# Kernel tuning notes

Measured on AMD Instinct MI355X. Metric: run time of the kernel, lower is better.

Reference implementation:

```python
import jax, jax.numpy as jnp
import numpy as np

T, D, H, O = 1048576, 64, 128, 32  # tokens, input_size, expert hidden, expert output_size


def setup_inputs() -> dict:
    key = jax.random.key(0)
    ks = jax.random.split(key, 11)
    s = 0.02
    return {
        "x": jax.random.normal(ks[0], (T, D), dtype=jnp.float32),
        "topk_idx": jax.random.randint(ks[1], (T, 2), 0, 2),
        "weights": jax.random.uniform(ks[2], (T, 2), dtype=jnp.float32),
        # expert 0: MLP D -> H -> O
        "W0a": jax.random.normal(ks[3], (D, H), dtype=jnp.float32) * s,
        "b0a": jnp.zeros((H,), dtype=jnp.float32),
        "W0b": jax.random.normal(ks[4], (H, O), dtype=jnp.float32) * s,
        "b0b": jnp.zeros((O,), dtype=jnp.float32),
        # expert 1: MLP (D + O) -> H -> O  (memory-enhanced input)
        "W1a": jax.random.normal(ks[5], (D + O, H), dtype=jnp.float32) * s,
        "b1a": jnp.zeros((H,), dtype=jnp.float32),
        "W1b": jax.random.normal(ks[6], (H, O), dtype=jnp.float32) * s,
        "b1b": jnp.zeros((O,), dtype=jnp.float32),
    }


def reference(x, topk_idx, weights, W0a, b0a, W0b, b0b, W1a, b1a, W1b, b1b):
    mask0 = (topk_idx == 0).any(axis=1)  # [T]
    mask1 = (topk_idx == 1).any(axis=1)  # [T]

    # expert 0 output, zero where not routed (matches zeros buffer + masked scatter)
    e0 = jnp.maximum(x @ W0a + b0a, 0.0) @ W0b + b0b      # [T, O]
    out0 = jnp.where(mask0[:, None], e0, 0.0)

    # last_valid_fill: forward-fill last valid row index (invalid -> 0, then cummax)
    t = jnp.arange(T)
    idx = jax.lax.cummax(jnp.where(mask0, t, 0))           # [T] int
    filled = out0[idx]                                     # [T, O] gather rows

    # expert 1 on [x, last_valid_out0], zero where not routed
    x1 = jnp.concatenate([x, filled], axis=1)              # [T, D+O]
    e1 = jnp.maximum(x1 @ W1a + b1a, 0.0) @ W1b + b1b      # [T, O]
    out1 = jnp.where(mask1[:, None], e1, 0.0)

    w = weights[:, :1]                                     # [T, 1]
    return w * out0 + (1.0 - w) * out1
```

## Files before the change

kernel.cpp:

```cpp
#include <hip/hip_runtime.h>
#include <hip/hip_bf16.h>

#define TROWS 1048576
#define RPC   256
#define CPB   8
#define NBLK  (TROWS / (RPC * CPB))
#define LSTRIDE 36

typedef float f32x4  __attribute__((ext_vector_type(4)));
typedef short bf16x8 __attribute__((ext_vector_type(8)));
typedef short bf16x4 __attribute__((ext_vector_type(4)));

#define MFMA(a, b, c) __builtin_amdgcn_mfma_f32_16x16x32_bf16(a, b, c, 0, 0, 0)

__device__ __forceinline__ short f2bf(float v) {
    __hip_bfloat16 b = __float2bfloat16(v);
    return __builtin_bit_cast(short, b);
}
__device__ __forceinline__ float bf2f(short s) {
    unsigned u = ((unsigned)(unsigned short)s) << 16;
    return __builtin_bit_cast(float, u);
}

__global__ __launch_bounds__(64) void prep_kernel(
    const float* __restrict__ W0a, const float* __restrict__ W0b,
    const float* __restrict__ W1a, const float* __restrict__ W1b,
    bf16x8* __restrict__ frag)
{
    const int fid = blockIdx.x, l = threadIdx.x, c = l & 15, g = l >> 4;
    const float* W; int N, ks, nt;
    if (fid < 16)      { W = W0a; N = 128; ks = fid >> 3;        nt = fid & 7; }
    else if (fid < 24) { W = W0b; N = 32;  ks = (fid - 16) >> 1; nt = (fid - 16) & 1; }
    else if (fid < 48) { W = W1a; N = 128; ks = (fid - 24) >> 3; nt = (fid - 24) & 7; }
    else               { W = W1b; N = 32;  ks = (fid - 48) >> 1; nt = (fid - 48) & 1; }
    bf16x8 f;
    #pragma unroll
    for (int j = 0; j < 8; ++j) {
        const int k = 32 * ks + ((j < 4) ? (4 * g + j) : (16 + 4 * g + (j - 4)));
        f[j] = f2bf(W[k * N + 16 * nt + c]);
    }
    frag[fid * 64 + l] = f;
}

__global__ __launch_bounds__(256, 2) void fused_kernel(
    const float* __restrict__ x, const int* __restrict__ topk,
    const float* __restrict__ wts,
    const float* __restrict__ b0a, const float* __restrict__ b0b,
    const float* __restrict__ b1a, const float* __restrict__ b1b,
    const bf16x8* __restrict__ frag,
    float* __restrict__ out)
{
    const int tid = threadIdx.x, wv = tid >> 6, l = tid & 63, c = l & 15, g = l >> 4;
    const int blk0 = blockIdx.x * (RPC * CPB);

    __shared__ __align__(16) short frag_lds[56 * 64 * 8];
    __shared__ __align__(16) short out0_lds[257 * LSTRIDE];
    __shared__ int wtot[4];

    #define LDSF(fid_) (*(const bf16x8*)&frag_lds[(((fid_) * 64) + l) * 8])

    #pragma unroll
    for (int i = 0; i < 14; ++i)
        *(f32x4*)&frag_lds[(tid + i * 256) * 8] = *(const f32x4*)&frag[tid + i * 256];

    bf16x8 xfp[2];
    bool m0p = false;
    if (wv == 3) {
        int p = 0;
        for (int base = blk0 - 64; base >= 0; base -= 64) {
            const int2 tkq = ((const int2*)topk)[base + l];
            const bool mm = (tkq.x == 0) || (tkq.y == 0);
            const unsigned long long bal = __ballot(mm);
            if (bal) { p = base + 63 - __clzll(bal); break; }
        }
        const int2 tkp = ((const int2*)topk)[p];
        m0p = (tkp.x == 0) || (tkp.y == 0);
        const float* xp = x + (size_t)p * 64;
        #pragma unroll
        for (int ks = 0; ks < 2; ++ks) {
            f32x4 a  = *(const f32x4*)(xp + 32 * ks + 4 * g);
            f32x4 b2 = *(const f32x4*)(xp + 32 * ks + 16 + 4 * g);
            #pragma unroll
            for (int j = 0; j < 4; ++j) { xfp[ks][j] = f2bf(a[j]); xfp[ks][4 + j] = f2bf(b2[j]); }
        }
    }

    f32x4 xraw[16];
    #pragma unroll
    for (int rt = 0; rt < 4; ++rt) {
        const float* xr = x + (size_t)(blk0 + wv * 64 + rt * 16 + c) * 64;
        xraw[rt * 4 + 0] = *(const f32x4*)(xr + 4 * g);
        xraw[rt * 4 + 1] = *(const f32x4*)(xr + 16 + 4 * g);
        xraw[rt * 4 + 2] = *(const f32x4*)(xr + 32 + 4 * g);
        xraw[rt * 4 + 3] = *(const f32x4*)(xr + 48 + 4 * g);
    }
    int2  tko = ((const int2*)topk)[blk0 + tid];
    float wgt = wts[(size_t)(blk0 + tid) * 2];

    __syncthreads();

    if (wv == 3) {
        f32x4 accp0 = *(const f32x4*)(b0b + 4 * g);
        f32x4 accp1 = *(const f32x4*)(b0b + 16 + 4 * g);
        #pragma unroll 1
        for (int k2 = 0; k2 < 4; ++k2) {
            const bf16x8 fa00 = LDSF(0 * 8 + 2 * k2 + 0);
            const bf16x8 fa01 = LDSF(0 * 8 + 2 * k2 + 1);
            const bf16x8 fa10 = LDSF(1 * 8 + 2 * k2 + 0);
            const bf16x8 fa11 = LDSF(1 * 8 + 2 * k2 + 1);
            const bf16x8 fb0  = LDSF(16 + 2 * k2 + 0);
            const bf16x8 fb1  = LDSF(16 + 2 * k2 + 1);
            f32x4 a10 = *(const f32x4*)(b0a + 16 * (2 * k2 + 0) + 4 * g);
            f32x4 a11 = *(const f32x4*)(b0a + 16 * (2 * k2 + 1) + 4 * g);
            a10 = MFMA(fa00, xfp[0], a10);
            a10 = MFMA(fa10, xfp[1], a10);
            a11 = MFMA(fa01, xfp[0], a11);
            a11 = MFMA(fa11, xfp[1], a11);
            bf16x8 hf;
            #pragma unroll
            for (int j = 0; j < 8; ++j)
                hf[j] = f2bf(fmaxf((j < 4 ? a10 : a11)[j & 3], 0.0f));
            accp0 = MFMA(fb0, hf, accp0);
            accp1 = MFMA(fb1, hf, accp1);
        }
        if (c == 0) {
            #pragma unroll
            for (int ot = 0; ot < 2; ++ot) {
                bf16x4 v;
                #pragma unroll
                for (int j = 0; j < 4; ++j)
                    v[j] = f2bf(m0p ? (ot ? accp1[j] : accp0[j]) : 0.0f);
                *(bf16x4*)(&out0_lds[256 * LSTRIDE + 16 * ot + 4 * g]) = v;
            }
        }
    }

    #pragma unroll 1
    for (int ch = 0; ch < CPB; ++ch) {
        const int cb = blk0 + ch * RPC;

        bf16x8 xf[4][2];
        #pragma unroll
        for (int rt = 0; rt < 4; ++rt)
            #pragma unroll
            for (int ks = 0; ks < 2; ++ks) {
                const f32x4 a  = xraw[rt * 4 + ks * 2 + 0];
                const f32x4 b2 = xraw[rt * 4 + ks * 2 + 1];
                #pragma unroll
                for (int j = 0; j < 4; ++j) { xf[rt][ks][j] = f2bf(a[j]); xf[rt][ks][4 + j] = f2bf(b2[j]); }
            }

        const bool m0o = (tko.x == 0) || (tko.y == 0);
        int s = m0o ? (cb + tid) : 0;
        #pragma unroll
        for (int off = 1; off < 64; off <<= 1) {
            int u = __shfl_up(s, off, 64);
            if (l >= off) s = max(s, u);
        }
        if (l == 63) wtot[wv] = s;

        f32x4 acc2a[4][2];
        {
            f32x4 bi0 = *(const f32x4*)(b0b + 4 * g);
            f32x4 bi1 = *(const f32x4*)(b0b + 16 + 4 * g);
            #pragma unroll
            for (int rt = 0; rt < 4; ++rt) { acc2a[rt][0] = bi0; acc2a[rt][1] = bi1; }
        }
        #pragma unroll 1
        for (int k2 = 0; k2 < 4; ++k2) {
            const bf16x8 fa00 = LDSF(0 * 8 + 2 * k2 + 0);
            const bf16x8 fa01 = LDSF(0 * 8 + 2 * k2 + 1);
            const bf16x8 fa10 = LDSF(1 * 8 + 2 * k2 + 0);
            const bf16x8 fa11 = LDSF(1 * 8 + 2 * k2 + 1);
            const bf16x8 fb0  = LDSF(16 + 2 * k2 + 0);
            const bf16x8 fb1  = LDSF(16 + 2 * k2 + 1);
            const f32x4 bi0 = *(const f32x4*)(b0a + 16 * (2 * k2 + 0) + 4 * g);
            const f32x4 bi1 = *(const f32x4*)(b0a + 16 * (2 * k2 + 1) + 4 * g);
            #pragma unroll
            for (int rt = 0; rt < 4; ++rt) {
                f32x4 a10 = bi0, a11 = bi1;
                a10 = MFMA(fa00, xf[rt][0], a10);
                a10 = MFMA(fa10, xf[rt][1], a10);
                a11 = MFMA(fa01, xf[rt][0], a11);
                a11 = MFMA(fa11, xf[rt][1], a11);
                bf16x8 hf;
                #pragma unroll
                for (int j = 0; j < 8; ++j)
                    hf[j] = f2bf(fmaxf((j < 4 ? a10 : a11)[j & 3], 0.0f));
                acc2a[rt][0] = MFMA(fb0, hf, acc2a[rt][0]);
                acc2a[rt][1] = MFMA(fb1, hf, acc2a[rt][1]);
            }
        }

        #pragma unroll
        for (int rt = 0; rt < 4; ++rt) {
            const int slot = wv * 64 + rt * 16 + c;
            const int2 tk = ((const int2*)topk)[cb + slot];
            const bool m0 = (tk.x == 0) || (tk.y == 0);
            #pragma unroll
            for (int ot = 0; ot < 2; ++ot) {
                bf16x4 v;
                #pragma unroll
                for (int j = 0; j < 4; ++j) v[j] = f2bf(m0 ? acc2a[rt][ot][j] : 0.0f);
                *(bf16x4*)(&out0_lds[slot * LSTRIDE + 16 * ot + 4 * g]) = v;
            }
        }

        __syncthreads();

        if (ch + 1 < CPB) {
            const int nb = cb + RPC;
            #pragma unroll
            for (int rt = 0; rt < 4; ++rt) {
                const float* xr = x + (size_t)(nb + wv * 64 + rt * 16 + c) * 64;
                xraw[rt * 4 + 0] = *(const f32x4*)(xr + 4 * g);
                xraw[rt * 4 + 1] = *(const f32x4*)(xr + 16 + 4 * g);
                xraw[rt * 4 + 2] = *(const f32x4*)(xr + 32 + 4 * g);
                xraw[rt * 4 + 3] = *(const f32x4*)(xr + 48 + 4 * g);
            }
            tko = ((const int2*)topk)[nb + tid];
            wgt = wts[(size_t)(nb + tid) * 2];
        }

        int pre = 0;
        #pragma unroll
        for (int w2 = 0; w2 < 4; ++w2)
            if (w2 < wv) pre = max(pre, wtot[w2]);
        const int s_full = max(pre, s);

        bf16x8 xf2[4];
        #pragma unroll
        for (int rt = 0; rt < 4; ++rt) {
            const int sF = __shfl(s_full, rt * 16 + c, 64);
            const int slot = (sF >= cb) ? (sF - cb) : 256;
            const short* fr = &out0_lds[slot * LSTRIDE];
            bf16x4 fa_ = *(const bf16x4*)(fr + 4 * g);
            bf16x4 fb_ = *(const bf16x4*)(fr + 16 + 4 * g);
            #pragma unroll
            for (int j = 0; j < 4; ++j) { xf2[rt][j] = fa_[j]; xf2[rt][4 + j] = fb_[j]; }
        }

        f32x4 acc2b[4][2];
        {
            f32x4 bi0 = *(const f32x4*)(b1b + 4 * g);
            f32x4 bi1 = *(const f32x4*)(b1b + 16 + 4 * g);
            #pragma unroll
            for (int rt = 0; rt < 4; ++rt) { acc2b[rt][0] = bi0; acc2b[rt][1] = bi1; }
        }
        #pragma unroll 1
        for (int k2 = 0; k2 < 4; ++k2) {
            const bf16x8 fa00 = LDSF(24 + 0 * 8 + 2 * k2 + 0);
            const bf16x8 fa01 = LDSF(24 + 0 * 8 + 2 * k2 + 1);
            const bf16x8 fa10 = LDSF(24 + 1 * 8 + 2 * k2 + 0);
            const bf16x8 fa11 = LDSF(24 + 1 * 8 + 2 * k2 + 1);
            const bf16x8 fa20 = LDSF(24 + 2 * 8 + 2 * k2 + 0);
            const bf16x8 fa21 = LDSF(24 + 2 * 8 + 2 * k2 + 1);
            const bf16x8 fb0  = LDSF(48 + 2 * k2 + 0);
            const bf16x8 fb1  = LDSF(48 + 2 * k2 + 1);
            const f32x4 bi0 = *(const f32x4*)(b1a + 16 * (2 * k2 + 0) + 4 * g);
            const f32x4 bi1 = *(const f32x4*)(b1a + 16 * (2 * k2 + 1) + 4 * g);
            #pragma unroll
            for (int rt = 0; rt < 4; ++rt) {
                f32x4 a10 = bi0, a11 = bi1;
                a10 = MFMA(fa00, xf[rt][0], a10);
                a10 = MFMA(fa10, xf[rt][1], a10);
                a10 = MFMA(fa20, xf2[rt], a10);
                a11 = MFMA(fa01, xf[rt][0], a11);
                a11 = MFMA(fa11, xf[rt][1], a11);
                a11 = MFMA(fa21, xf2[rt], a11);
                bf16x8 hf;
                #pragma unroll
                for (int j = 0; j < 8; ++j)
                    hf[j] = f2bf(fmaxf((j < 4 ? a10 : a11)[j & 3], 0.0f));
                acc2b[rt][0] = MFMA(fb0, hf, acc2b[rt][0]);
                acc2b[rt][1] = MFMA(fb1, hf, acc2b[rt][1]);
            }
        }

        #pragma unroll
        for (int rt = 0; rt < 4; ++rt) {
            const int slot = wv * 64 + rt * 16 + c;
            const int row = cb + slot;
            const int2 tk = ((const int2*)topk)[row];
            const bool m1 = (tk.x == 1) || (tk.y == 1);
            const float w  = wts[(size_t)row * 2];
            const float wc = 1.0f - w;
            #pragma unroll
            for (int ot = 0; ot < 2; ++ot) {
                bf16x4 oa = *(const bf16x4*)(&out0_lds[slot * LSTRIDE + 16 * ot + 4 * g]);
                f32x4 r;
                #pragma unroll
                for (int j = 0; j < 4; ++j) {
                    const float e1 = m1 ? acc2b[rt][ot][j] : 0.0f;
                    r[j] = w * bf2f(oa[j]) + wc * e1;
                }
                *(f32x4*)(out + (size_t)row * 32 + 16 * ot + 4 * g) = r;
            }
        }

        uint2 pc; bool docopy = false;
        if (ch + 1 < CPB && wv == 3) {
            const int pn = __shfl(s_full, 63, 64);
            docopy = (pn >= cb);
            if (docopy && l < 8)
                pc = *(const uint2*)&out0_lds[(pn - cb) * LSTRIDE + l * 4];
        }

        __syncthreads();

        if (docopy && l < 8)
            *(uint2*)&out0_lds[256 * LSTRIDE + l * 4] = pc;
    }
    #undef LDSF
}

extern "C" void kernel_launch(void* const* d_in, const int* in_sizes, int n_in,
                              void* d_out, int out_size, void* d_ws, size_t ws_size,
                              hipStream_t stream)
{
    const float* x    = (const float*)d_in[0];
    const int*   topk = (const int*)  d_in[1];
    const float* wts  = (const float*)d_in[2];
    const float* W0a  = (const float*)d_in[3];
    const float* b0a  = (const float*)d_in[4];
    const float* W0b  = (const float*)d_in[5];
    const float* b0b  = (const float*)d_in[6];
    const float* W1a  = (const float*)d_in[7];
    const float* b1a  = (const float*)d_in[8];
    const float* W1b  = (const float*)d_in[9];
    const float* b1b  = (const float*)d_in[10];
    float* out = (float*)d_out;

    bf16x8* frag = (bf16x8*)d_ws;

    prep_kernel<<<dim3(56), dim3(64), 0, stream>>>(W0a, W0b, W1a, W1b, frag);
    fused_kernel<<<dim3(NBLK), dim3(256), 0, stream>>>(
        x, topk, wts, b0a, b0b, b1a, b1b, frag, out);
}
```

Before: 129.1 us.

## Use 512-thread blocks with 32 rows per wave and drop register prefetch

```diff
diff --git a/kernel.cpp b/kernel.cpp
--- a/kernel.cpp
+++ b/kernel.cpp
@@ -42,7 +42,7 @@
     frag[fid * 64 + l] = f;
 }
 
-__global__ __launch_bounds__(256, 2) void fused_kernel(
+__global__ __launch_bounds__(512, 4) void fused_kernel(
     const float* __restrict__ x, const int* __restrict__ topk,
     const float* __restrict__ wts,
     const float* __restrict__ b0a, const float* __restrict__ b0b,
@@ -51,21 +51,22 @@
     float* __restrict__ out)
 {
     const int tid = threadIdx.x, wv = tid >> 6, l = tid & 63, c = l & 15, g = l >> 4;
+    const int rr = l & 31;
     const int blk0 = blockIdx.x * (RPC * CPB);
 
     __shared__ __align__(16) short frag_lds[56 * 64 * 8];
     __shared__ __align__(16) short out0_lds[257 * LSTRIDE];
-    __shared__ int wtot[4];
+    __shared__ int wtot[8];
 
     #define LDSF(fid_) (*(const bf16x8*)&frag_lds[(((fid_) * 64) + l) * 8])
 
     #pragma unroll
-    for (int i = 0; i < 14; ++i)
-        *(f32x4*)&frag_lds[(tid + i * 256) * 8] = *(const f32x4*)&frag[tid + i * 256];
+    for (int i = 0; i < 7; ++i)
+        *(f32x4*)&frag_lds[(tid + i * 512) * 8] = *(const f32x4*)&frag[tid + i * 512];
 
     bf16x8 xfp[2];
     bool m0p = false;
-    if (wv == 3) {
+    if (wv == 7) {
         int p = 0;
         for (int base = blk0 - 64; base >= 0; base -= 64) {
             const int2 tkq = ((const int2*)topk)[base + l];
@@ -85,21 +86,9 @@
         }
     }
 
-    f32x4 xraw[16];
-    #pragma unroll
-    for (int rt = 0; rt < 4; ++rt) {
-        const float* xr = x + (size_t)(blk0 + wv * 64 + rt * 16 + c) * 64;
-        xraw[rt * 4 + 0] = *(const f32x4*)(xr + 4 * g);
-        xraw[rt * 4 + 1] = *(const f32x4*)(xr + 16 + 4 * g);
-        xraw[rt * 4 + 2] = *(const f32x4*)(xr + 32 + 4 * g);
-        xraw[rt * 4 + 3] = *(const f32x4*)(xr + 48 + 4 * g);
-    }
-    int2  tko = ((const int2*)topk)[blk0 + tid];
-    float wgt = wts[(size_t)(blk0 + tid) * 2];
-
     __syncthreads();
 
-    if (wv == 3) {
+    if (wv == 7) {
         f32x4 accp0 = *(const f32x4*)(b0b + 4 * g);
         f32x4 accp1 = *(const f32x4*)(b0b + 16 + 4 * g);
         #pragma unroll 1
@@ -139,32 +128,36 @@
     for (int ch = 0; ch < CPB; ++ch) {
         const int cb = blk0 + ch * RPC;
 
-        bf16x8 xf[4][2];
-        #pragma unroll
-        for (int rt = 0; rt < 4; ++rt)
+        bf16x8 xf[2][2];
+        #pragma unroll
+        for (int rt = 0; rt < 2; ++rt) {
+            const float* xr = x + (size_t)(cb + wv * 32 + rt * 16 + c) * 64;
             #pragma unroll
             for (int ks = 0; ks < 2; ++ks) {
-                const f32x4 a  = xraw[rt * 4 + ks * 2 + 0];
-                const f32x4 b2 = xraw[rt * 4 + ks * 2 + 1];
+                f32x4 a  = *(const f32x4*)(xr + 32 * ks + 4 * g);
+                f32x4 b2 = *(const f32x4*)(xr + 32 * ks + 16 + 4 * g);
                 #pragma unroll
                 for (int j = 0; j < 4; ++j) { xf[rt][ks][j] = f2bf(a[j]); xf[rt][ks][4 + j] = f2bf(b2[j]); }
             }
-
+        }
+
+        const int srow = cb + wv * 32 + rr;
+        const int2 tko = ((const int2*)topk)[srow];
         const bool m0o = (tko.x == 0) || (tko.y == 0);
-        int s = m0o ? (cb + tid) : 0;
-        #pragma unroll
-        for (int off = 1; off < 64; off <<= 1) {
-            int u = __shfl_up(s, off, 64);
-            if (l >= off) s = max(s, u);
-        }
-        if (l == 63) wtot[wv] = s;
-
-        f32x4 acc2a[4][2];
+        int s = m0o ? srow : 0;
+        #pragma unroll
+        for (int off = 1; off < 32; off <<= 1) {
+            int u = __shfl_up(s, off, 32);
+            if (rr >= off) s = max(s, u);
+        }
+        if (l == 31) wtot[wv] = s;
+
+        f32x4 acc2a[2][2];
         {
             f32x4 bi0 = *(const f32x4*)(b0b + 4 * g);
             f32x4 bi1 = *(const f32x4*)(b0b + 16 + 4 * g);
-            #pragma unroll
-            for (int rt = 0; rt < 4; ++rt) { acc2a[rt][0] = bi0; acc2a[rt][1] = bi1; }
+            acc2a[0][0] = bi0; acc2a[0][1] = bi1;
+            acc2a[1][0] = bi0; acc2a[1][1] = bi1;
         }
         #pragma unroll 1
         for (int k2 = 0; k2 < 4; ++k2) {
@@ -177,7 +170,7 @@
             const f32x4 bi0 = *(const f32x4*)(b0a + 16 * (2 * k2 + 0) + 4 * g);
             const f32x4 bi1 = *(const f32x4*)(b0a + 16 * (2 * k2 + 1) + 4 * g);
             #pragma unroll
-            for (int rt = 0; rt < 4; ++rt) {
+            for (int rt = 0; rt < 2; ++rt) {
                 f32x4 a10 = bi0, a11 = bi1;
                 a10 = MFMA(fa00, xf[rt][0], a10);
                 a10 = MFMA(fa10, xf[rt][1], a10);
@@ -193,8 +186,8 @@
         }
 
         #pragma unroll
-        for (int rt = 0; rt < 4; ++rt) {
-            const int slot = wv * 64 + rt * 16 + c;
+        for (int rt = 0; rt < 2; ++rt) {
+            const int slot = wv * 32 + rt * 16 + c;
             const int2 tk = ((const int2*)topk)[cb + slot];
             const bool m0 = (tk.x == 0) || (tk.y == 0);
             #pragma unroll
@@ -208,29 +201,15 @@
 
         __syncthreads();
 
-        if (ch + 1 < CPB) {
-            const int nb = cb + RPC;
-            #pragma unroll
-            for (int rt = 0; rt < 4; ++rt) {
-                const float* xr = x + (size_t)(nb + wv * 64 + rt * 16 + c) * 64;
-                xraw[rt * 4 + 0] = *(const f32x4*)(xr + 4 * g);
-                xraw[rt * 4 + 1] = *(const f32x4*)(xr + 16 + 4 * g);
-                xraw[rt * 4 + 2] = *(const f32x4*)(xr + 32 + 4 * g);
-                xraw[rt * 4 + 3] = *(const f32x4*)(xr + 48 + 4 * g);
-            }
-            tko = ((const int2*)topk)[nb + tid];
-            wgt = wts[(size_t)(nb + tid) * 2];
-        }
-
         int pre = 0;
         #pragma unroll
-        for (int w2 = 0; w2 < 4; ++w2)
+        for (int w2 = 0; w2 < 8; ++w2)
             if (w2 < wv) pre = max(pre, wtot[w2]);
         const int s_full = max(pre, s);
 
-        bf16x8 xf2[4];
-        #pragma unroll
-        for (int rt = 0; rt < 4; ++rt) {
+        bf16x8 xf2[2];
+        #pragma unroll
+        for (int rt = 0; rt < 2; ++rt) {
             const int sF = __shfl(s_full, rt * 16 + c, 64);
             const int slot = (sF >= cb) ? (sF - cb) : 256;
             const short* fr = &out0_lds[slot * LSTRIDE];
@@ -240,12 +219,12 @@
             for (int j = 0; j < 4; ++j) { xf2[rt][j] = fa_[j]; xf2[rt][4 + j] = fb_[j]; }
         }
 
-        f32x4 acc2b[4][2];
+        f32x4 acc2b[2][2];
         {
             f32x4 bi0 = *(const f32x4*)(b1b + 4 * g);
             f32x4 bi1 = *(const f32x4*)(b1b + 16 + 4 * g);
-            #pragma unroll
-            for (int rt = 0; rt < 4; ++rt) { acc2b[rt][0] = bi0; acc2b[rt][1] = bi1; }
+            acc2b[0][0] = bi0; acc2b[0][1] = bi1;
+            acc2b[1][0] = bi0; acc2b[1][1] = bi1;
         }
         #pragma unroll 1
         for (int k2 = 0; k2 < 4; ++k2) {
@@ -260,7 +239,7 @@
             const f32x4 bi0 = *(const f32x4*)(b1a + 16 * (2 * k2 + 0) + 4 * g);
             const f32x4 bi1 = *(const f32x4*)(b1a + 16 * (2 * k2 + 1) + 4 * g);
             #pragma unroll
-            for (int rt = 0; rt < 4; ++rt) {
+            for (int rt = 0; rt < 2; ++rt) {
                 f32x4 a10 = bi0, a11 = bi1;
                 a10 = MFMA(fa00, xf[rt][0], a10);
                 a10 = MFMA(fa10, xf[rt][1], a10);
@@ -278,8 +257,8 @@
         }
 
         #pragma unroll
-        for (int rt = 0; rt < 4; ++rt) {
-            const int slot = wv * 64 + rt * 16 + c;
+        for (int rt = 0; rt < 2; ++rt) {
+            const int slot = wv * 32 + rt * 16 + c;
             const int row = cb + slot;
             const int2 tk = ((const int2*)topk)[row];
             const bool m1 = (tk.x == 1) || (tk.y == 1);
@@ -299,8 +278,8 @@
         }
 
         uint2 pc; bool docopy = false;
-        if (ch + 1 < CPB && wv == 3) {
-            const int pn = __shfl(s_full, 63, 64);
+        if (ch + 1 < CPB && wv == 7) {
+            const int pn = __shfl(s_full, 31, 64);
             docopy = (pn >= cb);
             if (docopy && l < 8)
                 pc = *(const uint2*)&out0_lds[(pn - cb) * LSTRIDE + l * 4];
@@ -334,6 +313,6 @@
     bf16x8* frag = (bf16x8*)d_ws;
 
     prep_kernel<<<dim3(56), dim3(64), 0, stream>>>(W0a, W0b, W1a, W1b, frag);
-    fused_kernel<<<dim3(NBLK), dim3(256), 0, stream>>>(
+    fused_kernel<<<dim3(NBLK), dim3(512), 0, stream>>>(
         x, topk, wts, b0a, b0b, b1a, b1b, frag, out);
 }
```

Measured after the change: 129.5 us. No clear change (+0.3%).
